# Kernel tuning notes

Measured on AMD Instinct MI355X. Metric: run time of the kernel, lower is better.

Reference implementation:

```python
import jax, jax.numpy as jnp
import numpy as np


def setup_inputs() -> dict:
    key = jax.random.key(0)
    k1, k2, k3 = jax.random.split(key, 3)
    B, S_TOT, HD = 2, 4096, 1024
    return {
        "q": jax.random.normal(k1, (B, S_TOT, HD), dtype=jnp.float32),
        "k": jax.random.normal(k2, (B, S_TOT, HD), dtype=jnp.float32),
        "v": jax.random.normal(k3, (B, S_TOT, HD), dtype=jnp.float32),
        "num_heads": 16,
        "num_shots": 4,
        "per_g": 64,
    }


def reference(q, k, v, num_heads, num_shots, per_g):
    # Equal-length shots: shot_latent_indices = [0, L, 2L, ..., s_tot] per batch.
    b, s_tot, hd = q.shape
    d = hd // num_heads
    L = s_tot // num_shots  # local shot length
    scale = 1.0 / jnp.sqrt(jnp.asarray(d, q.dtype))

    # [b, S, L, H, D]
    qs = q.reshape(b, num_shots, L, num_heads, d)
    ks = k.reshape(b, num_shots, L, num_heads, d)
    vs = v.reshape(b, num_shots, L, num_heads, d)

    # Global pool: first per_g tokens of each shot ('firstk'), shared by all shots.
    kg = ks[:, :, :per_g].reshape(b, num_shots * per_g, num_heads, d)  # [b, G, H, D]
    vg = vs[:, :, :per_g].reshape(b, num_shots * per_g, num_heads, d)

    # Block-local scores [b,S,H,L,L] and shared-global scores [b,S,H,L,G]
    s_loc = jnp.einsum("bsqhd,bskhd->bshqk", qs, ks) * scale
    s_glb = jnp.einsum("bsqhd,bghd->bshqg", qs, kg) * scale
    logits = jnp.concatenate([s_loc, s_glb], axis=-1)  # [b,S,H,L,L+G]
    p = jax.nn.softmax(logits, axis=-1)

    o_loc = jnp.einsum("bshqk,bskhd->bsqhd", p[..., :L], vs)
    o_glb = jnp.einsum("bshqg,bghd->bsqhd", p[..., L:], vg)
    out = (o_loc + o_glb).reshape(b, s_tot, hd)
    return out
```

## Files before the change

### kernel.cpp

```cpp
#include <hip/hip_runtime.h>
#include <hip/hip_bf16.h>

#define S_TOT 4096
#define HDIM  1024
#define NH    16
#define DH    64
#define L_    1024
#define NT    19

using bf16x8 = __attribute__((ext_vector_type(8))) short;
using f32x16 = __attribute__((ext_vector_type(16))) float;
using i32x4  = __attribute__((ext_vector_type(4))) int;

typedef const __attribute__((address_space(1))) unsigned int* gp1_t;
typedef __attribute__((address_space(3))) unsigned int* lp3_t;

__device__ __forceinline__ short f2bf(float f) {
    union { float f; unsigned u; } x; x.f = f;
    unsigned r = x.u + 0x7FFFu + ((x.u >> 16) & 1u);
    return (short)(r >> 16);
}

__device__ __forceinline__ unsigned cvt_pk_bf16(float lo, float hi) {
    unsigned r;
    asm("v_cvt_pk_bf16_f32 %0, %1, %2" : "=v"(r) : "v"(lo), "v"(hi));
    return r;
}

__device__ __forceinline__ float exp2_fast(float x) {
#if __has_builtin(__builtin_amdgcn_exp2f)
    return __builtin_amdgcn_exp2f(x);
#else
    return exp2f(x);
#endif
}

__device__ __forceinline__ void gload16(const void* g, void* l) {
    __builtin_amdgcn_global_load_lds((gp1_t)g, (lp3_t)(unsigned long)(l), 16, 0, 0);
}

__global__ __launch_bounds__(256) void prep_kv(
    const float* __restrict__ kf, const float* __restrict__ vf,
    short* __restrict__ kb, short* __restrict__ vb)
{
    __shared__ short st[64 * 70];
    const int bid = blockIdx.x, tid = threadIdx.x;
    if (bid < 1024) {
        const int gid = bid * 256 + tid;
        #pragma unroll
        for (int it = 0; it < 2; ++it) {
            size_t e = ((size_t)gid + (size_t)it * 262144) * 16;
            #pragma unroll
            for (int half = 0; half < 2; ++half) {
                float4 a = *(const float4*)(kf + e + half * 8);
                float4 c = *(const float4*)(kf + e + half * 8 + 4);
                bf16x8 r;
                r[0]=f2bf(a.x); r[1]=f2bf(a.y); r[2]=f2bf(a.z); r[3]=f2bf(a.w);
                r[4]=f2bf(c.x); r[5]=f2bf(c.y); r[6]=f2bf(c.z); r[7]=f2bf(c.w);
                *(bf16x8*)(kb + e + half * 8) = r;
            }
        }
    } else {
        const int vbid = bid - 1024;
        const int stile = vbid & 63, ht = (vbid >> 6) & 15, b = vbid >> 10;
        const int rt = tid >> 2, q4 = tid & 3;
        const float* src = vf + ((size_t)(b * S_TOT + stile * 64 + rt)) * HDIM + ht * 64 + q4 * 16;
        short* dst = st + rt * 70 + q4 * 16;
        #pragma unroll
        for (int i = 0; i < 4; ++i) {
            float4 x = *(const float4*)(src + i * 4);
            dst[i*4+0] = f2bf(x.x); dst[i*4+1] = f2bf(x.y);
            dst[i*4+2] = f2bf(x.z); dst[i*4+3] = f2bf(x.w);
        }
        __syncthreads();
        const int orow = tid >> 2, oq = tid & 3;
        bf16x8 o0, o1;
        #pragma unroll
        for (int j = 0; j < 8; ++j) o0[j] = st[(oq * 16 + j) * 70 + orow];
        #pragma unroll
        for (int j = 0; j < 8; ++j) o1[j] = st[(oq * 16 + 8 + j) * 70 + orow];
        short* dst2 = vb + ((size_t)((b * NH + ht) * 64 + orow)) * S_TOT + stile * 64 + oq * 16;
        *(bf16x8*)dst2 = o0;
        *(bf16x8*)(dst2 + 8) = o1;
    }
}

__global__ __launch_bounds__(512, 2) void attn_kernel(
    const float* __restrict__ qf, const short* __restrict__ kb,
    const short* __restrict__ vb, float* __restrict__ out)
{
    __shared__ __align__(16) char smem[49152];
    const int tid  = threadIdx.x;
    const int wave = tid >> 6, lane = tid & 63;
    const int hi   = lane >> 5, q32 = lane & 31;

    const int bidhw = blockIdx.x;
    const int bid = ((bidhw & 7) << 6) | (bidhw >> 3);
    const int qt = bid & 3, h = (bid >> 2) & 15, s = (bid >> 6) & 3, b = bid >> 8;

    const float CSC = 0.125f * 1.4426950408889634f;
    const float* qp = qf + ((size_t)(b*S_TOT + s*L_ + qt*256 + wave*32 + q32)) * HDIM
                         + h * DH + hi * 8;
    bf16x8 qv[4];
    #pragma unroll
    for (int d = 0; d < 4; ++d) {
        float4 x0 = *(const float4*)(qp + d * 16);
        float4 x1 = *(const float4*)(qp + d * 16 + 4);
        i32x4 u;
        u[0] = (int)cvt_pk_bf16(x0.x * CSC, x0.y * CSC);
        u[1] = (int)cvt_pk_bf16(x0.z * CSC, x0.w * CSC);
        u[2] = (int)cvt_pk_bf16(x1.x * CSC, x1.y * CSC);
        u[3] = (int)cvt_pk_bf16(x1.z * CSC, x1.w * CSC);
        qv[d] = __builtin_bit_cast(bf16x8, u);
    }

    const int cid = wave * 64 + lane;
    const int row = cid >> 3;
    const int lch = (cid & 7) ^ (row & 7);
    const int krow = (row & 0x33) | ((row & 4) << 1) | ((row & 8) >> 1);
    const size_t ko = (size_t)krow * 2048 + (lch << 4);
    const size_t vo = (size_t)row  * 8192 + (lch << 4);
    const char* kbase = (const char*)kb + ((size_t)b * S_TOT) * 2048 + h * 128;
    const char* vbase = (const char*)vb + ((size_t)(b * NH + h)) * (64ull * 8192);

    auto abs_tile_of = [&](int t) -> int {
        if (t < 16) return s * 16 + t;
        int g = t - 16; if (g >= s) ++g;
        return g * 16;
    };
    auto stage = [&](int t, int bo) {
        const int at = abs_tile_of(t);
        const char* kp = kbase + (size_t)at * 131072;
        const char* vp = vbase + (size_t)at * 128;
        char* dK = smem + bo + wave * 1024;
        gload16(kp + ko, dK);
        gload16(vp + vo, dK + 8192);
    };

    int qc[4];
    #pragma unroll
    for (int i = 0; i < 4; ++i)
        qc[i] = q32 * 128 + (((i * 2 + hi) ^ (q32 & 7)) << 4);

    f32x16 zro;
    #pragma unroll
    for (int r = 0; r < 16; ++r) zro[r] = 0.f;
    f32x16 acc0 = zro, acc1 = zro;
    float ps = 0.f;

    stage(0, 0);
    stage(1, 16384);
    asm volatile("s_waitcnt vmcnt(0)" ::: "memory");

    int rd = 0, nx = 16384, st = 32768;
    for (int t = 0; t < NT; ++t) {
        __builtin_amdgcn_sched_barrier(0);
        __builtin_amdgcn_s_barrier();
        __builtin_amdgcn_sched_barrier(0);

        if (t + 2 < NT) stage(t + 2, st);

        const float bias = (t == 0) ? 1.0f : 0.0f;
        const char* sb = smem + rd;

        f32x16 sA, sB;
        {
            __builtin_amdgcn_s_setprio(1);
            bf16x8 a0 = *(const bf16x8*)(sb + qc[0]);
            bf16x8 b0 = *(const bf16x8*)(sb + 4096 + qc[0]);
            sA = __builtin_amdgcn_mfma_f32_32x32x16_bf16(a0, qv[0], zro, 0,0,0);
            sB = __builtin_amdgcn_mfma_f32_32x32x16_bf16(b0, qv[0], zro, 0,0,0);
            bf16x8 a1 = *(const bf16x8*)(sb + qc[1]);
            bf16x8 b1 = *(const bf16x8*)(sb + 4096 + qc[1]);
            sA = __builtin_amdgcn_mfma_f32_32x32x16_bf16(a1, qv[1], sA, 0,0,0);
            sB = __builtin_amdgcn_mfma_f32_32x32x16_bf16(b1, qv[1], sB, 0,0,0);
            bf16x8 a2 = *(const bf16x8*)(sb + qc[2]);
            bf16x8 b2 = *(const bf16x8*)(sb + 4096 + qc[2]);
            sA = __builtin_amdgcn_mfma_f32_32x32x16_bf16(a2, qv[2], sA, 0,0,0);
            sB = __builtin_amdgcn_mfma_f32_32x32x16_bf16(b2, qv[2], sB, 0,0,0);
            bf16x8 a3 = *(const bf16x8*)(sb + qc[3]);
            bf16x8 b3 = *(const bf16x8*)(sb + 4096 + qc[3]);
            sA = __builtin_amdgcn_mfma_f32_32x32x16_bf16(a3, qv[3], sA, 0,0,0);
            sB = __builtin_amdgcn_mfma_f32_32x32x16_bf16(b3, qv[3], sB, 0,0,0);
            __builtin_amdgcn_s_setprio(0);
        }

        #pragma unroll
        for (int r = 0; r < 16; ++r) { float p = exp2_fast(sA[r] + bias); sA[r] = p; ps += p; }
        #pragma unroll
        for (int r = 0; r < 16; ++r) { float p = exp2_fast(sB[r] + bias); sB[r] = p; ps += p; }

        bf16x8 pf0, pf1, pf2, pf3;
        {
            i32x4 u;
            u[0]=(int)cvt_pk_bf16(sA[0],sA[1]);  u[1]=(int)cvt_pk_bf16(sA[2],sA[3]);
            u[2]=(int)cvt_pk_bf16(sA[4],sA[5]);  u[3]=(int)cvt_pk_bf16(sA[6],sA[7]);
            pf0 = __builtin_bit_cast(bf16x8, u);
            u[0]=(int)cvt_pk_bf16(sA[8],sA[9]);  u[1]=(int)cvt_pk_bf16(sA[10],sA[11]);
            u[2]=(int)cvt_pk_bf16(sA[12],sA[13]);u[3]=(int)cvt_pk_bf16(sA[14],sA[15]);
            pf1 = __builtin_bit_cast(bf16x8, u);
            u[0]=(int)cvt_pk_bf16(sB[0],sB[1]);  u[1]=(int)cvt_pk_bf16(sB[2],sB[3]);
            u[2]=(int)cvt_pk_bf16(sB[4],sB[5]);  u[3]=(int)cvt_pk_bf16(sB[6],sB[7]);
            pf2 = __builtin_bit_cast(bf16x8, u);
            u[0]=(int)cvt_pk_bf16(sB[8],sB[9]);  u[1]=(int)cvt_pk_bf16(sB[10],sB[11]);
            u[2]=(int)cvt_pk_bf16(sB[12],sB[13]);u[3]=(int)cvt_pk_bf16(sB[14],sB[15]);
            pf3 = __builtin_bit_cast(bf16x8, u);
        }

        {
            __builtin_amdgcn_s_setprio(1);
            bf16x8 v00 = *(const bf16x8*)(sb + 8192  + qc[0]);
            bf16x8 v10 = *(const bf16x8*)(sb + 12288 + qc[0]);
            acc0 = __builtin_amdgcn_mfma_f32_32x32x16_bf16(v00, pf0, acc0, 0,0,0);
            acc1 = __builtin_amdgcn_mfma_f32_32x32x16_bf16(v10, pf0, acc1, 0,0,0);
            bf16x8 v01 = *(const bf16x8*)(sb + 8192  + qc[1]);
            bf16x8 v11 = *(const bf16x8*)(sb + 12288 + qc[1]);
            acc0 = __builtin_amdgcn_mfma_f32_32x32x16_bf16(v01, pf1, acc0, 0,0,0);
            acc1 = __builtin_amdgcn_mfma_f32_32x32x16_bf16(v11, pf1, acc1, 0,0,0);
            bf16x8 v02 = *(const bf16x8*)(sb + 8192  + qc[2]);
            bf16x8 v12 = *(const bf16x8*)(sb + 12288 + qc[2]);
            acc0 = __builtin_amdgcn_mfma_f32_32x32x16_bf16(v02, pf2, acc0, 0,0,0);
            acc1 = __builtin_amdgcn_mfma_f32_32x32x16_bf16(v12, pf2, acc1, 0,0,0);
            bf16x8 v03 = *(const bf16x8*)(sb + 8192  + qc[3]);
            bf16x8 v13 = *(const bf16x8*)(sb + 12288 + qc[3]);
            acc0 = __builtin_amdgcn_mfma_f32_32x32x16_bf16(v03, pf3, acc0, 0,0,0);
            acc1 = __builtin_amdgcn_mfma_f32_32x32x16_bf16(v13, pf3, acc1, 0,0,0);
            __builtin_amdgcn_s_setprio(0);
        }

        if (t + 1 < NT) {
            if (t + 2 < NT) { asm volatile("s_waitcnt vmcnt(2)" ::: "memory"); }
            else            { asm volatile("s_waitcnt vmcnt(0)" ::: "memory"); }
        }
        int tmp = rd; rd = nx; nx = st; st = tmp;
    }

    float tot = ps + __shfl_xor(ps, 32);
    float inv = 1.0f / tot;
    const size_t orow = (size_t)(b*S_TOT + s*L_ + qt*256 + wave*32 + q32);
    float* op = out + orow * HDIM + h * DH;
    #pragma unroll
    for (int m = 0; m < 4; ++m) {
        float4 w0, w1;
        w0.x = acc0[4*m+0]*inv; w0.y = acc0[4*m+1]*inv;
        w0.z = acc0[4*m+2]*inv; w0.w = acc0[4*m+3]*inv;
        *(float4*)(op + 8*m + 4*hi) = w0;
        w1.x = acc1[4*m+0]*inv; w1.y = acc1[4*m+1]*inv;
        w1.z = acc1[4*m+2]*inv; w1.w = acc1[4*m+3]*inv;
        *(float4*)(op + 32 + 8*m + 4*hi) = w1;
    }
}

extern "C" void kernel_launch(void* const* d_in, const int* in_sizes, int n_in,
                              void* d_out, int out_size, void* d_ws, size_t ws_size,
                              hipStream_t stream) {
    const float* q = (const float*)d_in[0];
    const float* k = (const float*)d_in[1];
    const float* v = (const float*)d_in[2];
    char* ws = (char*)d_ws;
    short* kbuf = (short*)(ws);
    short* vbuf = (short*)(ws + (16u << 20));
    prep_kv<<<dim3(3072), dim3(256), 0, stream>>>(k, v, kbuf, vbuf);
    attn_kernel<<<dim3(512), dim3(512), 0, stream>>>(q, kbuf, vbuf, (float*)d_out);
}
```

Before: 73.27 us.

## Software-pipeline PV matmul of previous tile with QK of current tile

Defers the P·V MFMA block for each tile to the next iteration, issuing it right after the current tile's QK MFMAs, so matrix work overlaps the exp/convert softmax phase. LDS grows to four 16KB ring buffers so the previous tile's V stays resident while two tiles ahead are prefetched. A final epilogue runs the last tile's PV. The larger shared memory footprint could reduce occupancy, and it adds register pressure from keeping P fragments live across iterations.

```diff
diff --git a/kernel.cpp b/kernel.cpp
--- a/kernel.cpp
+++ b/kernel.cpp
@@ -89,7 +89,7 @@
     const float* __restrict__ qf, const short* __restrict__ kb,
     const short* __restrict__ vb, float* __restrict__ out)
 {
-    __shared__ __align__(16) char smem[49152];
+    __shared__ __align__(16) char smem[65536];
     const int tid  = threadIdx.x;
     const int wave = tid >> 6, lane = tid & 63;
     const int hi   = lane >> 5, q32 = lane & 31;
@@ -147,21 +147,24 @@
     for (int r = 0; r < 16; ++r) zro[r] = 0.f;
     f32x16 acc0 = zro, acc1 = zro;
     float ps = 0.f;
+    bf16x8 pf0, pf1, pf2, pf3;
+    { i32x4 z; z[0]=0; z[1]=0; z[2]=0; z[3]=0;
+      pf0 = __builtin_bit_cast(bf16x8, z); pf1 = pf0; pf2 = pf0; pf3 = pf0; }
 
     stage(0, 0);
     stage(1, 16384);
     asm volatile("s_waitcnt vmcnt(0)" ::: "memory");
 
-    int rd = 0, nx = 16384, st = 32768;
     for (int t = 0; t < NT; ++t) {
         __builtin_amdgcn_sched_barrier(0);
         __builtin_amdgcn_s_barrier();
         __builtin_amdgcn_sched_barrier(0);
 
-        if (t + 2 < NT) stage(t + 2, st);
-
+        if (t + 2 < NT) stage(t + 2, ((t + 2) & 3) << 14);
+
+        const char* sb  = smem + ((t & 3) << 14);
+        const char* vbp = smem + (((t + 3) & 3) << 14);
         const float bias = (t == 0) ? 1.0f : 0.0f;
-        const char* sb = smem + rd;
 
         f32x16 sA, sB;
         {
@@ -182,6 +185,25 @@
             bf16x8 b3 = *(const bf16x8*)(sb + 4096 + qc[3]);
             sA = __builtin_amdgcn_mfma_f32_32x32x16_bf16(a3, qv[3], sA, 0,0,0);
             sB = __builtin_amdgcn_mfma_f32_32x32x16_bf16(b3, qv[3], sB, 0,0,0);
+
+            if (t > 0) {
+                bf16x8 v00 = *(const bf16x8*)(vbp + 8192  + qc[0]);
+                bf16x8 v10 = *(const bf16x8*)(vbp + 12288 + qc[0]);
+                acc0 = __builtin_amdgcn_mfma_f32_32x32x16_bf16(v00, pf0, acc0, 0,0,0);
+                acc1 = __builtin_amdgcn_mfma_f32_32x32x16_bf16(v10, pf0, acc1, 0,0,0);
+                bf16x8 v01 = *(const bf16x8*)(vbp + 8192  + qc[1]);
+                bf16x8 v11 = *(const bf16x8*)(vbp + 12288 + qc[1]);
+                acc0 = __builtin_amdgcn_mfma_f32_32x32x16_bf16(v01, pf1, acc0, 0,0,0);
+                acc1 = __builtin_amdgcn_mfma_f32_32x32x16_bf16(v11, pf1, acc1, 0,0,0);
+                bf16x8 v02 = *(const bf16x8*)(vbp + 8192  + qc[2]);
+                bf16x8 v12 = *(const bf16x8*)(vbp + 12288 + qc[2]);
+                acc0 = __builtin_amdgcn_mfma_f32_32x32x16_bf16(v02, pf2, acc0, 0,0,0);
+                acc1 = __builtin_amdgcn_mfma_f32_32x32x16_bf16(v12, pf2, acc1, 0,0,0);
+                bf16x8 v03 = *(const bf16x8*)(vbp + 8192  + qc[3]);
+                bf16x8 v13 = *(const bf16x8*)(vbp + 12288 + qc[3]);
+                acc0 = __builtin_amdgcn_mfma_f32_32x32x16_bf16(v03, pf3, acc0, 0,0,0);
+                acc1 = __builtin_amdgcn_mfma_f32_32x32x16_bf16(v13, pf3, acc1, 0,0,0);
+            }
             __builtin_amdgcn_s_setprio(0);
         }
 
@@ -190,7 +212,6 @@
         #pragma unroll
         for (int r = 0; r < 16; ++r) { float p = exp2_fast(sB[r] + bias); sB[r] = p; ps += p; }
 
-        bf16x8 pf0, pf1, pf2, pf3;
         {
             i32x4 u;
             u[0]=(int)cvt_pk_bf16(sA[0],sA[1]);  u[1]=(int)cvt_pk_bf16(sA[2],sA[3]);
@@ -207,32 +228,30 @@
             pf3 = __builtin_bit_cast(bf16x8, u);
         }
 
-        {
-            __builtin_amdgcn_s_setprio(1);
-            bf16x8 v00 = *(const bf16x8*)(sb + 8192  + qc[0]);
-            bf16x8 v10 = *(const bf16x8*)(sb + 12288 + qc[0]);
-            acc0 = __builtin_amdgcn_mfma_f32_32x32x16_bf16(v00, pf0, acc0, 0,0,0);
-            acc1 = __builtin_amdgcn_mfma_f32_32x32x16_bf16(v10, pf0, acc1, 0,0,0);
-            bf16x8 v01 = *(const bf16x8*)(sb + 8192  + qc[1]);
-            bf16x8 v11 = *(const bf16x8*)(sb + 12288 + qc[1]);
-            acc0 = __builtin_amdgcn_mfma_f32_32x32x16_bf16(v01, pf1, acc0, 0,0,0);
-            acc1 = __builtin_amdgcn_mfma_f32_32x32x16_bf16(v11, pf1, acc1, 0,0,0);
-            bf16x8 v02 = *(const bf16x8*)(sb + 8192  + qc[2]);
-            bf16x8 v12 = *(const bf16x8*)(sb + 12288 + qc[2]);
-            acc0 = __builtin_amdgcn_mfma_f32_32x32x16_bf16(v02, pf2, acc0, 0,0,0);
-            acc1 = __builtin_amdgcn_mfma_f32_32x32x16_bf16(v12, pf2, acc1, 0,0,0);
-            bf16x8 v03 = *(const bf16x8*)(sb + 8192  + qc[3]);
-            bf16x8 v13 = *(const bf16x8*)(sb + 12288 + qc[3]);
-            acc0 = __builtin_amdgcn_mfma_f32_32x32x16_bf16(v03, pf3, acc0, 0,0,0);
-            acc1 = __builtin_amdgcn_mfma_f32_32x32x16_bf16(v13, pf3, acc1, 0,0,0);
-            __builtin_amdgcn_s_setprio(0);
-        }
-
-        if (t + 1 < NT) {
-            if (t + 2 < NT) { asm volatile("s_waitcnt vmcnt(2)" ::: "memory"); }
-            else            { asm volatile("s_waitcnt vmcnt(0)" ::: "memory"); }
-        }
-        int tmp = rd; rd = nx; nx = st; st = tmp;
+        if (t + 2 < NT) { asm volatile("s_waitcnt vmcnt(2)" ::: "memory"); }
+        else           { asm volatile("s_waitcnt vmcnt(0)" ::: "memory"); }
+    }
+
+    {
+        const char* vbp = smem + (((NT - 1) & 3) << 14);
+        __builtin_amdgcn_s_setprio(1);
+        bf16x8 v00 = *(const bf16x8*)(vbp + 8192  + qc[0]);
+        bf16x8 v10 = *(const bf16x8*)(vbp + 12288 + qc[0]);
+        acc0 = __builtin_amdgcn_mfma_f32_32x32x16_bf16(v00, pf0, acc0, 0,0,0);
+        acc1 = __builtin_amdgcn_mfma_f32_32x32x16_bf16(v10, pf0, acc1, 0,0,0);
+        bf16x8 v01 = *(const bf16x8*)(vbp + 8192  + qc[1]);
+        bf16x8 v11 = *(const bf16x8*)(vbp + 12288 + qc[1]);
+        acc0 = __builtin_amdgcn_mfma_f32_32x32x16_bf16(v01, pf1, acc0, 0,0,0);
+        acc1 = __builtin_amdgcn_mfma_f32_32x32x16_bf16(v11, pf1, acc1, 0,0,0);
+        bf16x8 v02 = *(const bf16x8*)(vbp + 8192  + qc[2]);
+        bf16x8 v12 = *(const bf16x8*)(vbp + 12288 + qc[2]);
+        acc0 = __builtin_amdgcn_mfma_f32_32x32x16_bf16(v02, pf2, acc0, 0,0,0);
+        acc1 = __builtin_amdgcn_mfma_f32_32x32x16_bf16(v12, pf2, acc1, 0,0,0);
+        bf16x8 v03 = *(const bf16x8*)(vbp + 8192  + qc[3]);
+        bf16x8 v13 = *(const bf16x8*)(vbp + 12288 + qc[3]);
+        acc0 = __builtin_amdgcn_mfma_f32_32x32x16_bf16(v03, pf3, acc0, 0,0,0);
+        acc1 = __builtin_amdgcn_mfma_f32_32x32x16_bf16(v13, pf3, acc1, 0,0,0);
+        __builtin_amdgcn_s_setprio(0);
     }
 
     float tot = ps + __shfl_xor(ps, 32);
```

After: 73.64 us. No clear change (+0.5%).
